# Kernel optimization log

Measured on AMD Instinct MI355X. Metric: run time of the kernel, lower is better.

The kernel has to match this reference:

```python
import jax, jax.numpy as jnp
import numpy as np
from jax import lax

DN = ('NCHW', 'OIHW', 'NCHW')

def conv(x, w, b, stride):
    y = lax.conv_general_dilated(x, w, window_strides=(stride, stride),
                                 padding='VALID', dimension_numbers=DN)
    return y + b[None, :, None, None]

def setup_inputs() -> dict:
    key = jax.random.key(0)
    ks = jax.random.split(key, 7)
    B = 4096
    def he(k, shape, fan_in):
        return jax.random.normal(k, shape, jnp.float32) * np.sqrt(2.0 / fan_in)
    return {
        'x':  jax.random.normal(ks[0], (B, 3, 48, 64), jnp.float32),
        'w1': he(ks[1], (32, 3, 8, 8), 3 * 8 * 8),
        'b1': jnp.zeros((32,), jnp.float32),
        'w2': he(ks[2], (64, 32, 3, 3), 32 * 3 * 3),
        'b2': jnp.zeros((64,), jnp.float32),
        'w3': he(ks[3], (64, 64, 3, 3), 64 * 3 * 3),
        'b3': jnp.zeros((64,), jnp.float32),
        'w4': he(ks[4], (512, 960), 960),
        'b4': jnp.zeros((512,), jnp.float32),
        'w5': he(ks[5], (2, 512), 512),
        'b5': jnp.zeros((2,), jnp.float32),
    }

def reference(x, w1, b1, w2, b2, w3, b3, w4, b4, w5, b5):
    # conv1 (k8 s4): [B,3,48,64] -> [B,32,11,15]
    x1 = conv(x, w1, b1, 4)
    # side reduction (torch code does this on CPU with python loops):
    # sum over batch and channel dims of pre-ReLU activation, divided by 32
    ave1 = jnp.sum(x1, axis=(0, 1)) / 32.0          # [11,15]
    x2 = jax.nn.relu(x1)
    # conv2 (k3 s2): -> [B,64,5,7]
    x3 = conv(x2, w2, b2, 2)
    ave2 = jnp.sum(x3, axis=(0, 1)) / 64.0          # [5,7]
    x4 = jax.nn.relu(x3)
    # conv3 (k3 s1): -> [B,64,3,5]
    x5 = conv(x4, w3, b3, 1)
    ave3 = jnp.sum(x5, axis=(0, 1)) / 64.0          # [3,5]
    x6 = jax.nn.relu(x5)
    # fc head: flatten (C,H,W order, matching torch) -> 960 -> 512 -> 2
    h = x6.reshape(x6.shape[0], -1)                 # [B,960]
    h = jax.nn.relu(h @ w4.T + b4)
    out = h @ w5.T + b5                             # [B,2]
    return out, ave1, ave2, ave3
```

## Files before the change

kernel.cpp:

```cpp
#include <hip/hip_runtime.h>
#include <hip/hip_bf16.h>

#define BATCH 4096

typedef __attribute__((ext_vector_type(8))) short short8;
typedef __attribute__((ext_vector_type(4))) float f32x4;

#define MFMA_BF16 __builtin_amdgcn_mfma_f32_16x16x32_bf16

__device__ __forceinline__ float frelu(float v) { return v > 0.f ? v : 0.f; }
__device__ __forceinline__ unsigned short f2bf(float f) {
    return __builtin_bit_cast(unsigned short, __float2bfloat16(f));
}
__device__ __forceinline__ short8 cvt8(const float* p) {
    float4 a = *(const float4*)p;
    float4 b = *(const float4*)(p + 4);
    short8 r;
    r[0] = (short)f2bf(a.x); r[1] = (short)f2bf(a.y); r[2] = (short)f2bf(a.z); r[3] = (short)f2bf(a.w);
    r[4] = (short)f2bf(b.x); r[5] = (short)f2bf(b.y); r[6] = (short)f2bf(b.z); r[7] = (short)f2bf(b.w);
    return r;
}

__global__ __launch_bounds__(256) void prep_kernel(const float* __restrict__ w2, const float* __restrict__ w3,
                                                   const float* __restrict__ w4, const float* __restrict__ b5,
                                                   unsigned short* __restrict__ w2p, unsigned short* __restrict__ w3p,
                                                   unsigned short* __restrict__ w4p, float* __restrict__ out) {
    int idx = blockIdx.x * 256 + threadIdx.x;
    if (idx < 18432) {
        int oc = idx / 288, k = idx % 288;
        int khw = k / 32, ic = k % 32;
        w2p[idx] = f2bf(w2[oc * 288 + ic * 9 + khw]);
    } else if (idx < 55296) {
        int j = idx - 18432;
        int oc = j / 576, k = j % 576;
        int khw = k / 64, ic = k % 64;
        w3p[j] = f2bf(w3[oc * 576 + ic * 9 + khw]);
    } else if (idx < 546816) {
        int j = idx - 55296;
        int n = j / 960, k = j % 960;
        int pos = k / 64, oc = k % 64;
        w4p[j] = f2bf(w4[n * 960 + oc * 15 + pos]);
    } else if (idx < 555008) {
        int j = idx - 546816;
        out[j] = b5[j & 1];
    } else if (idx < 555223) {
        out[8192 + (idx - 555008)] = 0.f;
    }
}

__global__ __launch_bounds__(256) void conv1_mfma(const float* __restrict__ x,
                                                  const float* __restrict__ w1, const float* __restrict__ b1,
                                                  unsigned short* __restrict__ x2, float* __restrict__ red1) {
    __shared__ float xs[3 * 48 * 68];
    __shared__ float red[176];
    const int img = blockIdx.x;
    const int tid = threadIdx.x;
    const int wave = tid >> 6, lane = tid & 63;
    const int col = lane & 15, quad = lane >> 4;

    const float4* xg = (const float4*)(x + (size_t)img * 9216);
    for (int i = tid; i < 2304; i += 256) {
        int row = i >> 4, seg = i & 15;
        *(float4*)(xs + row * 68 + seg * 4) = xg[row * 16 + seg];
    }
    if (tid < 176) red[tid] = 0.f;

    short8 Bf[2][6];
    #pragma unroll
    for (int nt = 0; nt < 2; ++nt) {
        const int oc = nt * 16 + col;
        #pragma unroll
        for (int c = 0; c < 6; ++c)
            Bf[nt][c] = cvt8(w1 + oc * 192 + c * 32 + quad * 8);
    }
    const float bias0 = b1[col], bias1 = b1[col + 16];
    __syncthreads();

    #pragma unroll
    for (int ti = 0; ti < 3; ++ti) {
        const int t = wave + ti * 4;
        if (t >= 11) break;
        const int posA = t * 16 + col;
        const int pm = posA < 165 ? posA : 164;
        const int oh = pm / 15, ow = pm % 15;
        f32x4 acc0 = {0.f, 0.f, 0.f, 0.f}, acc1 = {0.f, 0.f, 0.f, 0.f};
        #pragma unroll
        for (int c = 0; c < 6; ++c) {
            const int ic = c >> 1;
            const int kh = (c & 1) * 4 + quad;
            const float* ap = xs + ic * 3264 + (oh * 4 + kh) * 68 + ow * 4;
            short8 af = cvt8(ap);
            acc0 = MFMA_BF16(af, Bf[0][c], acc0, 0, 0, 0);
            acc1 = MFMA_BF16(af, Bf[1][c], acc1, 0, 0, 0);
        }
        #pragma unroll
        for (int r = 0; r < 4; ++r) {
            const int pr = t * 16 + quad * 4 + r;
            float v0 = acc0[r] + bias0;
            float v1 = acc1[r] + bias1;
            float s = v0 + v1;
            s += __shfl_xor(s, 1); s += __shfl_xor(s, 2);
            s += __shfl_xor(s, 4); s += __shfl_xor(s, 8);
            if (pr < 165) {
                if (col == 0) atomicAdd(&red[pr], s);
                unsigned short* dst = x2 + ((size_t)img * 165 + pr) * 32;
                dst[col]      = f2bf(frelu(v0));
                dst[col + 16] = f2bf(frelu(v1));
            }
        }
    }
    __syncthreads();
    if (tid < 176) red1[(size_t)tid * 4096 + img] = red[tid];
}

__global__ __launch_bounds__(256) void reduce1_kernel(const float* __restrict__ red1, float* __restrict__ ave1) {
    const int pos = blockIdx.x;
    float s = 0.f;
    for (int i = threadIdx.x; i < 4096; i += 256) s += red1[(size_t)pos * 4096 + i];
    s += __shfl_down(s, 32); s += __shfl_down(s, 16); s += __shfl_down(s, 8);
    s += __shfl_down(s, 4);  s += __shfl_down(s, 2);  s += __shfl_down(s, 1);
    __shared__ float wsum[4];
    if ((threadIdx.x & 63) == 0) wsum[threadIdx.x >> 6] = s;
    __syncthreads();
    if (threadIdx.x == 0) ave1[pos] = (wsum[0] + wsum[1] + wsum[2] + wsum[3]) * 0.03125f;
}

__global__ __launch_bounds__(256) void conv2_mfma(const unsigned short* __restrict__ x2,
                                                  const unsigned short* __restrict__ w2p, const float* __restrict__ b2,
                                                  unsigned short* __restrict__ x4, float* __restrict__ ave2) {
    __shared__ unsigned short wl[64 * 296];
    __shared__ float red[35];
    const int tid = threadIdx.x;
    {
        const float4* src = (const float4*)w2p;
        for (int i = tid; i < 2304; i += 256) {
            int row = i / 36, off = i % 36;
            *(float4*)((char*)wl + row * 592 + off * 16) = src[i];
        }
    }
    if (tid < 35) red[tid] = 0.f;
    __syncthreads();

    const int wave = tid >> 6, lane = tid & 63;
    const int col = lane & 15, quad = lane >> 4;
    const int tile0 = blockIdx.x * 8 + wave * 2;

    const unsigned short* abase[2];
    #pragma unroll
    for (int mi = 0; mi < 2; ++mi) {
        const int m = (tile0 + mi) * 16 + col;
        const int b = m / 35, pos = m % 35;
        const int oh = pos / 7, ow = pos % 7;
        abase[mi] = x2 + ((size_t)b * 165 + oh * 30 + ow * 2) * 32 + quad * 8;
    }
    f32x4 acc[2][4] = {};
    #pragma unroll
    for (int c = 0; c < 9; ++c) {
        const int kh = c / 3, kw = c % 3;
        short8 Bf[4];
        #pragma unroll
        for (int nt = 0; nt < 4; ++nt)
            Bf[nt] = *(const short8*)((const char*)wl + ((nt * 16 + col) * 296 + c * 32 + quad * 8) * 2);
        #pragma unroll
        for (int mi = 0; mi < 2; ++mi) {
            short8 af = *(const short8*)(abase[mi] + (kh * 15 + kw) * 32);
            #pragma unroll
            for (int nt = 0; nt < 4; ++nt)
                acc[mi][nt] = MFMA_BF16(af, Bf[nt], acc[mi][nt], 0, 0, 0);
        }
    }
    float bv[4];
    #pragma unroll
    for (int nt = 0; nt < 4; ++nt) bv[nt] = b2[nt * 16 + col];
    #pragma unroll
    for (int mi = 0; mi < 2; ++mi) {
        const int mrow0 = (tile0 + mi) * 16;
        #pragma unroll
        for (int r = 0; r < 4; ++r) {
            const int m = mrow0 + quad * 4 + r;
            const int b = m / 35, pos = m % 35;
            unsigned short* dst = x4 + ((size_t)b * 35 + pos) * 64;
            float s = 0.f;
            #pragma unroll
            for (int nt = 0; nt < 4; ++nt) {
                float v = acc[mi][nt][r] + bv[nt];
                s += v;
                dst[nt * 16 + col] = f2bf(frelu(v));
            }
            s += __shfl_xor(s, 1); s += __shfl_xor(s, 2); s += __shfl_xor(s, 4); s += __shfl_xor(s, 8);
            if (col == 0) atomicAdd(&red[pos], s);
        }
    }
    __syncthreads();
    if (tid < 35) atomicAdd(&ave2[tid], red[tid] * 0.015625f);
}

__global__ __launch_bounds__(256) void conv3_mfma(const unsigned short* __restrict__ x4,
                                                  const unsigned short* __restrict__ w3p, const float* __restrict__ b3,
                                                  unsigned short* __restrict__ x6, float* __restrict__ ave3) {
    __shared__ unsigned short wl[32 * 584];
    __shared__ float red[15];
    const int tid = threadIdx.x;
    const int oc0 = blockIdx.y * 32;
    {
        const float4* src = (const float4*)(w3p + (size_t)oc0 * 576);
        for (int i = tid; i < 2304; i += 256) {
            int row = i / 72, off = i % 72;
            *(float4*)((char*)wl + row * 1168 + off * 16) = src[i];
        }
    }
    if (tid < 15) red[tid] = 0.f;
    __syncthreads();

    const int wave = tid >> 6, lane = tid & 63;
    const int col = lane & 15, quad = lane >> 4;
    const int tile0 = blockIdx.x * 8 + wave * 2;

    const unsigned short* abase[2];
    #pragma unroll
    for (int mi = 0; mi < 2; ++mi) {
        const int m = (tile0 + mi) * 16 + col;
        const int b = m / 15, pos = m % 15;
        const int oh = pos / 5, ow = pos % 5;
        abase[mi] = x4 + ((size_t)b * 35 + oh * 7 + ow) * 64 + quad * 8;
    }
    f32x4 acc[2][2] = {};
    #pragma unroll
    for (int c = 0; c < 18; ++c) {
        const int khw = c >> 1, kh = khw / 3, kw = khw % 3;
        const int icoff = (c & 1) * 32;
        short8 Bf[2];
        #pragma unroll
        for (int nt = 0; nt < 2; ++nt)
            Bf[nt] = *(const short8*)((const char*)wl + ((nt * 16 + col) * 584 + c * 32 + quad * 8) * 2);
        #pragma unroll
        for (int mi = 0; mi < 2; ++mi) {
            short8 af = *(const short8*)(abase[mi] + (kh * 7 + kw) * 64 + icoff);
            #pragma unroll
            for (int nt = 0; nt < 2; ++nt)
                acc[mi][nt] = MFMA_BF16(af, Bf[nt], acc[mi][nt], 0, 0, 0);
        }
    }
    float bv[2];
    #pragma unroll
    for (int nt = 0; nt < 2; ++nt) bv[nt] = b3[oc0 + nt * 16 + col];
    #pragma unroll
    for (int mi = 0; mi < 2; ++mi) {
        const int mrow0 = (tile0 + mi) * 16;
        #pragma unroll
        for (int r = 0; r < 4; ++r) {
            const int m = mrow0 + quad * 4 + r;
            const int b = m / 15, pos = m % 15;
            unsigned short* dst = x6 + (size_t)b * 960 + pos * 64 + oc0;
            float s = 0.f;
            #pragma unroll
            for (int nt = 0; nt < 2; ++nt) {
                float v = acc[mi][nt][r] + bv[nt];
                s += v;
                dst[nt * 16 + col] = f2bf(frelu(v));
            }
            s += __shfl_xor(s, 1); s += __shfl_xor(s, 2); s += __shfl_xor(s, 4); s += __shfl_xor(s, 8);
            if (col == 0) atomicAdd(&red[pos], s);
        }
    }
    __syncthreads();
    if (tid < 15) atomicAdd(&ave3[tid], red[tid] * 0.015625f);
}

__global__ __launch_bounds__(256) void fc4_mfma(const unsigned short* __restrict__ x6,
                                                const unsigned short* __restrict__ w4p, const float* __restrict__ b4,
                                                const float* __restrict__ w5, float* __restrict__ out) {
    __shared__ unsigned short wl[32 * 968];
    const int tid = threadIdx.x;
    const int wave = tid >> 6, lane = tid & 63;
    const int col = lane & 15, quad = lane >> 4;
    const int m0 = blockIdx.x * 128;
    const int oc0 = blockIdx.y * 32;

    {
        const float4* src = (const float4*)(w4p + (size_t)oc0 * 960);
        for (int i = tid; i < 3840; i += 256) {
            int row = i / 120, seg = i % 120;
            *(float4*)((char*)wl + row * 1936 + seg * 16) = src[i];
        }
    }
    __syncthreads();

    const unsigned short* arow0 = x6 + (size_t)(m0 + wave * 32 + col) * 960 + quad * 8;
    const unsigned short* arow1 = arow0 + 16 * 960;
    f32x4 acc[2][2] = {};
    for (int c = 0; c < 30; ++c) {
        short8 Bf[2];
        #pragma unroll
        for (int nt = 0; nt < 2; ++nt)
            Bf[nt] = *(const short8*)((const char*)wl + ((nt * 16 + col) * 968 + c * 32 + quad * 8) * 2);
        short8 a0 = *(const short8*)(arow0 + c * 32);
        short8 a1 = *(const short8*)(arow1 + c * 32);
        #pragma unroll
        for (int nt = 0; nt < 2; ++nt) {
            acc[0][nt] = MFMA_BF16(a0, Bf[nt], acc[0][nt], 0, 0, 0);
            acc[1][nt] = MFMA_BF16(a1, Bf[nt], acc[1][nt], 0, 0, 0);
        }
    }
    float bv[2], w50[2], w51[2];
    #pragma unroll
    for (int nt = 0; nt < 2; ++nt) {
        const int oc = oc0 + nt * 16 + col;
        bv[nt] = b4[oc]; w50[nt] = w5[oc]; w51[nt] = w5[512 + oc];
    }
    #pragma unroll
    for (int mi = 0; mi < 2; ++mi) {
        #pragma unroll
        for (int r = 0; r < 4; ++r) {
            float l0 = 0.f, l1 = 0.f;
            #pragma unroll
            for (int nt = 0; nt < 2; ++nt) {
                float hh = frelu(acc[mi][nt][r] + bv[nt]);
                l0 += hh * w50[nt];
                l1 += hh * w51[nt];
            }
            l0 += __shfl_xor(l0, 1); l0 += __shfl_xor(l0, 2); l0 += __shfl_xor(l0, 4); l0 += __shfl_xor(l0, 8);
            l1 += __shfl_xor(l1, 1); l1 += __shfl_xor(l1, 2); l1 += __shfl_xor(l1, 4); l1 += __shfl_xor(l1, 8);
            if (col == 0) {
                const int gm = m0 + wave * 32 + mi * 16 + quad * 4 + r;
                atomicAdd(&out[gm * 2 + 0], l0);
                atomicAdd(&out[gm * 2 + 1], l1);
            }
        }
    }
}

extern "C" void kernel_launch(void* const* d_in, const int* in_sizes, int n_in,
                              void* d_out, int out_size, void* d_ws, size_t ws_size,
                              hipStream_t stream) {
    const float* x  = (const float*)d_in[0];
    const float* w1 = (const float*)d_in[1];
    const float* b1 = (const float*)d_in[2];
    const float* w2 = (const float*)d_in[3];
    const float* b2 = (const float*)d_in[4];
    const float* w3 = (const float*)d_in[5];
    const float* b3 = (const float*)d_in[6];
    const float* w4 = (const float*)d_in[7];
    const float* b4 = (const float*)d_in[8];
    const float* w5 = (const float*)d_in[9];
    const float* b5 = (const float*)d_in[10];
    float* out = (float*)d_out;

    unsigned short* ws = (unsigned short*)d_ws;
    unsigned short* x2  = ws;
    unsigned short* x4  = ws + 21626880;
    unsigned short* x6  = ws + 30801920;
    unsigned short* w2p = ws + 34734080;
    unsigned short* w3p = ws + 34752512;
    unsigned short* w4p = ws + 34789376;
    float* red1 = (float*)((char*)d_ws + 70561792);

    float* ave1 = out + 8192;
    float* ave2 = out + 8192 + 165;
    float* ave3 = out + 8192 + 200;

    prep_kernel<<<2169, 256, 0, stream>>>(w2, w3, w4, b5, w2p, w3p, w4p, out);
    conv1_mfma<<<BATCH, 256, 0, stream>>>(x, w1, b1, x2, red1);
    reduce1_kernel<<<165, 256, 0, stream>>>(red1, ave1);
    conv2_mfma<<<1120, 256, 0, stream>>>(x2, w2p, b2, x4, ave2);
    conv3_mfma<<<dim3(480, 2), 256, 0, stream>>>(x4, w3p, b3, x6, ave3);
    fc4_mfma<<<dim3(32, 16), 256, 0, stream>>>(x6, w4p, b4, w5, out);
}
```

Baseline: 379.6 us.

## Merge prep and reduce kernels into conv launches and stage conv1 input as bf16

The weight-repacking prep kernel becomes extra blocks appended to the conv1 grid, and the ave1 reduction becomes extra blocks appended to the conv2 grid. This removes two kernel launches and their serialization gaps. conv1 also converts the input tile to bf16 once while staging it into shared memory, which halves LDS use and removes the per-fragment float-to-bf16 conversion in the inner loop. The merged blocks must not depend on work from the same grid; the ave1 blocks read red1, which conv1 fully writes before conv2 starts, so this holds.

```diff
diff --git a/kernel.cpp b/kernel.cpp
--- a/kernel.cpp
+++ b/kernel.cpp
@@ -11,6 +11,9 @@
 __device__ __forceinline__ float frelu(float v) { return v > 0.f ? v : 0.f; }
 __device__ __forceinline__ unsigned short f2bf(float f) {
     return __builtin_bit_cast(unsigned short, __float2bfloat16(f));
+}
+__device__ __forceinline__ unsigned int pack2bf(float a, float b) {
+    return (unsigned int)f2bf(a) | ((unsigned int)f2bf(b) << 16);
 }
 __device__ __forceinline__ short8 cvt8(const float* p) {
     float4 a = *(const float4*)p;
@@ -20,38 +23,46 @@
     r[4] = (short)f2bf(b.x); r[5] = (short)f2bf(b.y); r[6] = (short)f2bf(b.z); r[7] = (short)f2bf(b.w);
     return r;
 }
-
-__global__ __launch_bounds__(256) void prep_kernel(const float* __restrict__ w2, const float* __restrict__ w3,
-                                                   const float* __restrict__ w4, const float* __restrict__ b5,
-                                                   unsigned short* __restrict__ w2p, unsigned short* __restrict__ w3p,
-                                                   unsigned short* __restrict__ w4p, float* __restrict__ out) {
-    int idx = blockIdx.x * 256 + threadIdx.x;
-    if (idx < 18432) {
-        int oc = idx / 288, k = idx % 288;
-        int khw = k / 32, ic = k % 32;
-        w2p[idx] = f2bf(w2[oc * 288 + ic * 9 + khw]);
-    } else if (idx < 55296) {
-        int j = idx - 18432;
-        int oc = j / 576, k = j % 576;
-        int khw = k / 64, ic = k % 64;
-        w3p[j] = f2bf(w3[oc * 576 + ic * 9 + khw]);
-    } else if (idx < 546816) {
-        int j = idx - 55296;
-        int n = j / 960, k = j % 960;
-        int pos = k / 64, oc = k % 64;
-        w4p[j] = f2bf(w4[n * 960 + oc * 15 + pos]);
-    } else if (idx < 555008) {
-        int j = idx - 546816;
-        out[j] = b5[j & 1];
-    } else if (idx < 555223) {
-        out[8192 + (idx - 555008)] = 0.f;
-    }
+__device__ __forceinline__ short8 lds_frag(const unsigned short* p) {
+    uint2 a = *(const uint2*)p;
+    uint2 b = *(const uint2*)(p + 4);
+    uint4 u = {a.x, a.y, b.x, b.y};
+    return __builtin_bit_cast(short8, u);
 }
 
 __global__ __launch_bounds__(256) void conv1_mfma(const float* __restrict__ x,
                                                   const float* __restrict__ w1, const float* __restrict__ b1,
-                                                  unsigned short* __restrict__ x2, float* __restrict__ red1) {
-    __shared__ float xs[3 * 48 * 68];
+                                                  const float* __restrict__ w2, const float* __restrict__ w3,
+                                                  const float* __restrict__ w4, const float* __restrict__ b5,
+                                                  unsigned short* __restrict__ x2, float* __restrict__ red1,
+                                                  unsigned short* __restrict__ w2p, unsigned short* __restrict__ w3p,
+                                                  unsigned short* __restrict__ w4p, float* __restrict__ out) {
+    if (blockIdx.x >= 4096) {
+        int idx = (blockIdx.x - 4096) * 256 + threadIdx.x;
+        if (idx < 18432) {
+            int oc = idx / 288, k = idx % 288;
+            int khw = k / 32, ic = k % 32;
+            w2p[idx] = f2bf(w2[oc * 288 + ic * 9 + khw]);
+        } else if (idx < 55296) {
+            int j = idx - 18432;
+            int oc = j / 576, k = j % 576;
+            int khw = k / 64, ic = k % 64;
+            w3p[j] = f2bf(w3[oc * 576 + ic * 9 + khw]);
+        } else if (idx < 546816) {
+            int j = idx - 55296;
+            int n = j / 960, k = j % 960;
+            int pos = k / 64, oc = k % 64;
+            w4p[j] = f2bf(w4[n * 960 + oc * 15 + pos]);
+        } else if (idx < 555008) {
+            int j = idx - 546816;
+            out[j] = b5[j & 1];
+        } else if (idx < 555223) {
+            out[8192 + (idx - 555008)] = 0.f;
+        }
+        return;
+    }
+
+    __shared__ unsigned short xs[144 * 68];
     __shared__ float red[176];
     const int img = blockIdx.x;
     const int tid = threadIdx.x;
@@ -61,7 +72,9 @@
     const float4* xg = (const float4*)(x + (size_t)img * 9216);
     for (int i = tid; i < 2304; i += 256) {
         int row = i >> 4, seg = i & 15;
-        *(float4*)(xs + row * 68 + seg * 4) = xg[row * 16 + seg];
+        float4 v = xg[i];
+        uint2 u = {pack2bf(v.x, v.y), pack2bf(v.z, v.w)};
+        *(uint2*)(xs + row * 68 + seg * 4) = u;
     }
     if (tid < 176) red[tid] = 0.f;
 
@@ -83,15 +96,19 @@
         const int posA = t * 16 + col;
         const int pm = posA < 165 ? posA : 164;
         const int oh = pm / 15, ow = pm % 15;
-        f32x4 acc0 = {0.f, 0.f, 0.f, 0.f}, acc1 = {0.f, 0.f, 0.f, 0.f};
+
+        short8 af[6];
         #pragma unroll
         for (int c = 0; c < 6; ++c) {
             const int ic = c >> 1;
             const int kh = (c & 1) * 4 + quad;
-            const float* ap = xs + ic * 3264 + (oh * 4 + kh) * 68 + ow * 4;
-            short8 af = cvt8(ap);
-            acc0 = MFMA_BF16(af, Bf[0][c], acc0, 0, 0, 0);
-            acc1 = MFMA_BF16(af, Bf[1][c], acc1, 0, 0, 0);
+            af[c] = lds_frag(xs + (ic * 48 + oh * 4 + kh) * 68 + ow * 4);
+        }
+        f32x4 acc0 = {0.f, 0.f, 0.f, 0.f}, acc1 = {0.f, 0.f, 0.f, 0.f};
+        #pragma unroll
+        for (int c = 0; c < 6; ++c) {
+            acc0 = MFMA_BF16(af[c], Bf[0][c], acc0, 0, 0, 0);
+            acc1 = MFMA_BF16(af[c], Bf[1][c], acc1, 0, 0, 0);
         }
         #pragma unroll
         for (int r = 0; r < 4; ++r) {
@@ -113,24 +130,24 @@
     if (tid < 176) red1[(size_t)tid * 4096 + img] = red[tid];
 }
 
-__global__ __launch_bounds__(256) void reduce1_kernel(const float* __restrict__ red1, float* __restrict__ ave1) {
-    const int pos = blockIdx.x;
-    float s = 0.f;
-    for (int i = threadIdx.x; i < 4096; i += 256) s += red1[(size_t)pos * 4096 + i];
-    s += __shfl_down(s, 32); s += __shfl_down(s, 16); s += __shfl_down(s, 8);
-    s += __shfl_down(s, 4);  s += __shfl_down(s, 2);  s += __shfl_down(s, 1);
-    __shared__ float wsum[4];
-    if ((threadIdx.x & 63) == 0) wsum[threadIdx.x >> 6] = s;
-    __syncthreads();
-    if (threadIdx.x == 0) ave1[pos] = (wsum[0] + wsum[1] + wsum[2] + wsum[3]) * 0.03125f;
-}
-
 __global__ __launch_bounds__(256) void conv2_mfma(const unsigned short* __restrict__ x2,
                                                   const unsigned short* __restrict__ w2p, const float* __restrict__ b2,
-                                                  unsigned short* __restrict__ x4, float* __restrict__ ave2) {
+                                                  unsigned short* __restrict__ x4, float* __restrict__ ave2,
+                                                  const float* __restrict__ red1, float* __restrict__ ave1) {
     __shared__ unsigned short wl[64 * 296];
     __shared__ float red[35];
     const int tid = threadIdx.x;
+    if (blockIdx.x >= 1120) {
+        const int pos = blockIdx.x - 1120;
+        float s = 0.f;
+        for (int i = tid; i < 4096; i += 256) s += red1[(size_t)pos * 4096 + i];
+        s += __shfl_down(s, 32); s += __shfl_down(s, 16); s += __shfl_down(s, 8);
+        s += __shfl_down(s, 4);  s += __shfl_down(s, 2);  s += __shfl_down(s, 1);
+        if ((tid & 63) == 0) red[tid >> 6] = s;
+        __syncthreads();
+        if (tid == 0) ave1[pos] = (red[0] + red[1] + red[2] + red[3]) * 0.03125f;
+        return;
+    }
     {
         const float4* src = (const float4*)w2p;
         for (int i = tid; i < 2304; i += 256) {
@@ -359,10 +376,9 @@
     float* ave2 = out + 8192 + 165;
     float* ave3 = out + 8192 + 200;
 
-    prep_kernel<<<2169, 256, 0, stream>>>(w2, w3, w4, b5, w2p, w3p, w4p, out);
-    conv1_mfma<<<BATCH, 256, 0, stream>>>(x, w1, b1, x2, red1);
-    reduce1_kernel<<<165, 256, 0, stream>>>(red1, ave1);
-    conv2_mfma<<<1120, 256, 0, stream>>>(x2, w2p, b2, x4, ave2);
+    conv1_mfma<<<4096 + 2169, 256, 0, stream>>>(x, w1, b1, w2, w3, w4, b5,
+                                                x2, red1, w2p, w3p, w4p, out);
+    conv2_mfma<<<1120 + 165, 256, 0, stream>>>(x2, w2p, b2, x4, ave2, red1, ave1);
     conv3_mfma<<<dim3(480, 2), 256, 0, stream>>>(x4, w3p, b3, x6, ave3);
     fc4_mfma<<<dim3(32, 16), 256, 0, stream>>>(x6, w4p, b4, w5, out);
 }
```

New measurement: 366.0 us. 3.6% less time.
